# Kernel tuning notes

Measured on AMD Instinct MI355X. Metric: run time of the kernel, lower is better.

Reference implementation:

```python
import jax, jax.numpy as jnp
import numpy as np

B, C, Q, T, D = 16, 6, 256, 256, 256
NUM_IDS = 300
IMG_H = IMG_W = 512


def setup_inputs() -> dict:
    key = jax.random.key(0)
    ks = jax.random.split(key, 8)
    det_tokens = jax.random.normal(ks[0], (B, C, Q, D), jnp.float32)
    det_scores = jax.random.uniform(ks[1], (B, C, Q), jnp.float32)
    det_boxes = jax.random.uniform(ks[2], (B, C, Q, 4), jnp.float32)
    assoc = jax.nn.softmax(jax.random.normal(ks[3], (B, C, Q, T), jnp.float32), axis=-1)
    cam_mask = jax.random.uniform(ks[4], (B, C)) < 0.9
    target_mask = jax.random.uniform(ks[5], (B, C, Q)) < 0.5
    ids = jax.random.randint(ks[6], (B, C, Q), 0, NUM_IDS)
    boxes = jax.random.uniform(ks[7], (B, C, Q, 4), jnp.float32) * IMG_W
    return {"det_tokens": det_tokens, "det_scores": det_scores, "det_boxes": det_boxes,
            "assoc": assoc, "boxes": boxes, "cam_mask": cam_mask,
            "target_mask": target_mask, "ids": ids, "img_h": IMG_H, "img_w": IMG_W}


def _masked_mean(x, m):
    w = m.astype(x.dtype)
    return (x * w).sum() / jnp.maximum(w.sum(), 1.0)


def _pack(ids, target_mask, cam_mask, q_count):
    # Vectorized version of _query_ids_from_targets: stable-compact valid targets
    # to the front of the query axis (preserves original order, as boolean indexing does).
    order = jnp.argsort(jnp.where(target_mask, 0, 1), axis=-1, stable=True)  # valid first
    sids = jnp.take_along_axis(ids, order, axis=-1)[..., :q_count]
    count = target_mask.sum(axis=-1)  # [B,C]
    qvalid = (jnp.arange(q_count)[None, None, :] < count[..., None]) & cam_mask[..., None]
    qids = jnp.where(qvalid, sids, -1)
    return qids, qvalid, order


def reference(det_tokens, det_scores, det_boxes, assoc, boxes, cam_mask, target_mask, ids, img_h, img_w):
    Bq, Cc, Qn, Tn = assoc.shape
    qids, qvalid, order = _pack(ids, target_mask, cam_mask, Qn)

    # det_norm
    det_norm = jnp.mean(det_tokens ** 2)

    # detector supervision (masked BCE on scores + masked L1 on boxes)
    norm = jnp.array([img_w, img_h, img_w, img_h], det_boxes.dtype)
    box_gt = boxes / norm  # [B,C,maxT,4]
    sboxes = jnp.take_along_axis(box_gt, order[..., None], axis=2)[:, :, :Qn]
    obj_target = qvalid.astype(det_scores.dtype)
    box_target = jnp.where(qvalid[..., None], jnp.clip(sboxes, 0.0, 1.0), 0.0)
    p = jnp.clip(det_scores, 1e-6, 1.0 - 1e-6)
    bce = -(obj_target * jnp.log(p) + (1.0 - obj_target) * jnp.log1p(-p))
    cam3 = jnp.broadcast_to(cam_mask[:, :, None], bce.shape)
    score_loss = _masked_mean(bce, cam3)
    box_loss = _masked_mean(jnp.abs(det_boxes - box_target),
                            jnp.broadcast_to(qvalid[..., None], det_boxes.shape))
    det_supervision = score_loss + box_loss

    # assoc entropy (masked by camera validity)
    logp_full = jnp.log(jnp.maximum(assoc, 1e-8))
    entropy = -(logp_full * assoc).sum(-1)  # [B,C,Q]
    assoc_entropy_loss = _masked_mean(entropy, jnp.broadcast_to(cam_mask[:, :, None], entropy.shape))

    # assoc supervised NLL over track slots
    slots = jnp.remainder(jnp.maximum(qids, 0), Tn)  # [B,C,Q]
    nll = -jnp.take_along_axis(logp_full, slots[..., None], axis=-1)[..., 0]
    assoc_pair_loss = _masked_mean(nll, qvalid)

    # cross-view consistency: broadcasted id-equality replaces quadruple python loop
    eq = qids[:, :, None, :, None] == qids[:, None, :, None, :]       # [B,c1,c2,q1,q2]
    pv = qvalid[:, :, None, :, None] & qvalid[:, None, :, None, :]
    tri = jnp.triu(jnp.ones((Cc, Cc), bool), 1)[None, :, :, None, None]  # c1 < c2
    M = (eq & pv & tri).astype(assoc.dtype)
    cnt = M.sum(-1)  # [B,c1,c2,q1]
    peer = jnp.einsum('bcdqp,bdpt->bcdqt', M, assoc) / jnp.maximum(cnt, 1.0)[..., None]
    ref = assoc[:, :, None, :, :]
    term = jnp.mean((ref - peer) ** 2, axis=-1)  # per-pair MSE over track slots
    assoc_consistency = _masked_mean(term, cnt > 0)

    total = det_norm + det_supervision + assoc_entropy_loss + assoc_pair_loss + assoc_consistency
    return total, det_norm, det_supervision, assoc_entropy_loss, assoc_pair_loss, assoc_consistency
```

## Files before the change

### kernel.cpp

```cpp
#include <hip/hip_runtime.h>
#include <math.h>

#define BB 16
#define CC 6
#define QQ 256
#define TT 256
#define DD 256
#define NPAIR 15
#define NBC (BB * CC)
#define BIG_BLOCKS (NBC * 16)
#define CONS_BLOCKS (BB * NPAIR * 4)
#define MAIN_BLOCKS (BIG_BLOCKS + CONS_BLOCKS)


__device__ __forceinline__ float block_sum256(float v, float* s_red) {
    #pragma unroll
    for (int off = 32; off > 0; off >>= 1) v += __shfl_xor(v, off, 64);
    __syncthreads();
    if ((threadIdx.x & 63) == 0) s_red[threadIdx.x >> 6] = v;
    __syncthreads();
    return s_red[0] + s_red[1] + s_red[2] + s_red[3];
}

__device__ __forceinline__ float2 block_sum256x2(float a, float b, float2* s_red2) {
    #pragma unroll
    for (int off = 32; off > 0; off >>= 1) {
        a += __shfl_xor(a, off, 64);
        b += __shfl_xor(b, off, 64);
    }
    __syncthreads();
    if ((threadIdx.x & 63) == 0) s_red2[threadIdx.x >> 6] = make_float2(a, b);
    __syncthreads();
    float2 r;
    r.x = s_red2[0].x + s_red2[1].x + s_red2[2].x + s_red2[3].x;
    r.y = s_red2[0].y + s_red2[1].y + s_red2[2].y + s_red2[3].y;
    return r;
}

__device__ __forceinline__ int read_bool(const void* p, int idx, int fmt) {
    if (fmt == 2) return ((const float*)p)[idx] != 0.0f;
    if (fmt == 1) return ((const unsigned char*)p)[idx] != 0;
    return ((const int*)p)[idx] != 0;
}

__global__ __launch_bounds__(256)
void k_pack(const float* __restrict__ det_scores,
            const float* __restrict__ det_boxes,
            const float* __restrict__ assoc,
            const float* __restrict__ boxes,
            const void* __restrict__ cam_raw,
            const void* __restrict__ tm_raw,
            const int* __restrict__ ids,
            const int* __restrict__ img_h_p,
            const int* __restrict__ img_w_p,
            unsigned char* __restrict__ cam_c,
            int* __restrict__ qids,
            float* __restrict__ packPart) {
    const int bc = blockIdx.x;
    const int t = threadIdx.x;
    const int lane = t & 63, wv = t >> 6;
    __shared__ int s_cf, s_cm, s_wsum[4];
    __shared__ int s_sids[QQ];
    __shared__ float s_red[4];

    if (t == 0) { s_cf = 0; s_cm = 0; }
    __syncthreads();
    {
        uint4 w = ((const uint4*)tm_raw)[t];
        unsigned int u4[4] = {w.x, w.y, w.z, w.w};
        int cf = 0, cm = 0;
        #pragma unroll
        for (int k = 0; k < 4; k++) {
            cf += ((u4[k] >> 24) == 0x3Fu);
            cm += ((u4[k] & 0xFFFFFF00u) != 0u);
        }
        if (cf) atomicAdd(&s_cf, cf);
        if (cm) atomicAdd(&s_cm, cm);
    }
    __syncthreads();
    const int fmt = (s_cf > 16) ? 2 : ((s_cm > 0) ? 1 : 0);

    const int cam = read_bool(cam_raw, bc, fmt);
    const int tm  = read_bool(tm_raw, bc * QQ + t, fmt);
    if (t == 0) cam_c[bc] = (unsigned char)cam;

    int v = tm;
    #pragma unroll
    for (int off = 1; off < 64; off <<= 1) {
        int u = __shfl_up(v, off, 64);
        if (lane >= off) v += u;
    }
    if (lane == 63) s_wsum[wv] = v;
    __syncthreads();
    const int count = s_wsum[0] + s_wsum[1] + s_wsum[2] + s_wsum[3];
    int woff = 0;
    #pragma unroll
    for (int k = 0; k < 3; k++) woff += (k < wv) ? s_wsum[k] : 0;
    const int excl = woff + v - tm;
    const int rank = tm ? excl : (count + (t - excl));

    s_sids[rank] = ids[bc * QQ + t];
    __syncthreads();

    const int j = t;
    const int qv = (j < count) && cam;
    const int qid = qv ? s_sids[j] : -1;
    qids[bc * QQ + j] = qid;

    float score_sum = 0.0f, box_sum = 0.0f, pair_sum = 0.0f;

    if (cam) {
        float p = det_scores[(size_t)bc * QQ + j];
        p = fminf(fmaxf(p, 1e-6f), 1.0f - 1e-6f);
        score_sum = (j < count) ? -__logf(p) : -__logf(1.0f - p);
    }
    if (qv) {
        int slot = qid & (TT - 1);
        float a = assoc[((size_t)bc * QQ + j) * TT + slot];
        pair_sum = -__logf(fmaxf(a, 1e-8f));
    }
    if (tm && cam) {
        const int jj = rank;
        const float iw = (float)img_w_p[0], ih = (float)img_h_p[0];
        const float* bx = boxes + ((size_t)bc * QQ + t) * 4;
        const float* db = det_boxes + ((size_t)bc * QQ + jj) * 4;
        float b0 = fminf(fmaxf(bx[0] / iw, 0.0f), 1.0f);
        float b1 = fminf(fmaxf(bx[1] / ih, 0.0f), 1.0f);
        float b2 = fminf(fmaxf(bx[2] / iw, 0.0f), 1.0f);
        float b3 = fminf(fmaxf(bx[3] / ih, 0.0f), 1.0f);
        box_sum = fabsf(db[0] - b0) + fabsf(db[1] - b1) +
                  fabsf(db[2] - b2) + fabsf(db[3] - b3);
    }

    float vs = block_sum256(score_sum, s_red);
    float vb = block_sum256(box_sum, s_red);
    float vp = block_sum256(pair_sum, s_red);
    if (t == 0) {
        float* row = packPart + bc * 8;
        row[0] = vs; row[1] = vb; row[2] = vp;
        row[3] = cam ? (float)count : 0.0f;
        row[4] = (float)cam;
    }
}

__global__ __launch_bounds__(256)
void k_main(const float4* __restrict__ tok, const float* __restrict__ assoc,
            const unsigned char* __restrict__ cam_c,
            const int* __restrict__ qids,
            float* __restrict__ bigPart, float* __restrict__ consPart) {
    const int blk = blockIdx.x;
    const int t = threadIdx.x, lane = t & 63, wv = t >> 6;
    __shared__ float2 s_red2[4];

    if (blk < BIG_BLOCKS) {
        const int bc = blk >> 4;
        const long base = (long)bc * 16384 + (long)(blk & 15) * 1024 + t;
        const float4* asc = (const float4*)assoc;

        float4 t0 = tok[base], t1 = tok[base + 256],
               t2 = tok[base + 512], t3 = tok[base + 768];
        float4 a0 = asc[base], a1 = asc[base + 256],
               a2 = asc[base + 512], a3 = asc[base + 768];
        const int cam = cam_c[bc];

        float ss = t0.x * t0.x + t0.y * t0.y + t0.z * t0.z + t0.w * t0.w
                 + t1.x * t1.x + t1.y * t1.y + t1.z * t1.z + t1.w * t1.w
                 + t2.x * t2.x + t2.y * t2.y + t2.z * t2.z + t2.w * t2.w
                 + t3.x * t3.x + t3.y * t3.y + t3.z * t3.z + t3.w * t3.w;

        float ent = 0.0f;
        if (cam) {
            ent -= a0.x * __logf(fmaxf(a0.x, 1e-8f)) + a0.y * __logf(fmaxf(a0.y, 1e-8f))
                 + a0.z * __logf(fmaxf(a0.z, 1e-8f)) + a0.w * __logf(fmaxf(a0.w, 1e-8f));
            ent -= a1.x * __logf(fmaxf(a1.x, 1e-8f)) + a1.y * __logf(fmaxf(a1.y, 1e-8f))
                 + a1.z * __logf(fmaxf(a1.z, 1e-8f)) + a1.w * __logf(fmaxf(a1.w, 1e-8f));
            ent -= a2.x * __logf(fmaxf(a2.x, 1e-8f)) + a2.y * __logf(fmaxf(a2.y, 1e-8f))
                 + a2.z * __logf(fmaxf(a2.z, 1e-8f)) + a2.w * __logf(fmaxf(a2.w, 1e-8f));
            ent -= a3.x * __logf(fmaxf(a3.x, 1e-8f)) + a3.y * __logf(fmaxf(a3.y, 1e-8f))
                 + a3.z * __logf(fmaxf(a3.z, 1e-8f)) + a3.w * __logf(fmaxf(a3.w, 1e-8f));
        }
        float2 r = block_sum256x2(ss, ent, s_red2);
        if (t == 0) { bigPart[blk * 2] = r.x; bigPart[blk * 2 + 1] = r.y; }
    } else {
        const int cb = blk - BIG_BLOCKS;
        const int qg = cb & 3;
        const int bp = cb >> 2;
        const int b = bp / NPAIR;
        int pi = bp % NPAIR;
        int c = 0, d = 1;
        {
            int k = pi;
            for (c = 0; c < CC - 1; c++) {
                int span = CC - 1 - c;
                if (k < span) { d = c + 1 + k; break; }
                k -= span;
            }
        }
        __shared__ int s_qc[64];
        __shared__ int s_qd[QQ];
        if (t < 64) s_qc[t] = qids[(b * CC + c) * QQ + qg * 64 + t];
        s_qd[t] = qids[(b * CC + d) * QQ + t];
        __syncthreads();

        const int qd0 = s_qd[lane];
        const int qd1 = s_qd[64 + lane];
        const int qd2 = s_qd[128 + lane];
        const int qd3 = s_qd[192 + lane];
        int idarr[16];
        #pragma unroll
        for (int qi = 0; qi < 16; qi++) idarr[qi] = s_qc[wv * 16 + qi];

        const float4* assoc_c = (const float4*)(assoc + (size_t)(b * CC + c) * QQ * TT);
        const float4* assoc_d = (const float4*)(assoc + (size_t)(b * CC + d) * QQ * TT);

        float tot = 0.0f;
        float nval = 0.0f;
        #pragma unroll 4
        for (int qi = 0; qi < 16; qi++) {
            const int id = idarr[qi];
            if (id < 0) continue;
            unsigned long long m0 = __ballot(qd0 == id);
            unsigned long long m1 = __ballot(qd1 == id);
            unsigned long long m2 = __ballot(qd2 == id);
            unsigned long long m3 = __ballot(qd3 == id);
            int cnt = __popcll(m0) + __popcll(m1) + __popcll(m2) + __popcll(m3);
            if (cnt == 0) continue;
            const int q = qg * 64 + wv * 16 + qi;
            float4 r = assoc_c[(size_t)q * (TT / 4) + lane];
            float ax = 0.0f, ay = 0.0f, az = 0.0f, aw = 0.0f;
            unsigned long long mm[4] = {m0, m1, m2, m3};
            #pragma unroll
            for (int kk = 0; kk < 4; kk++) {
                unsigned long long m = mm[kk];
                while (m) {
                    int p = kk * 64 + __builtin_ctzll(m);
                    m &= m - 1;
                    float4 vv = assoc_d[(size_t)p * (TT / 4) + lane];
                    ax += vv.x; ay += vv.y; az += vv.z; aw += vv.w;
                }
            }
            float inv = 1.0f / (float)cnt;
            float dx = r.x - ax * inv, dy = r.y - ay * inv;
            float dz = r.z - az * inv, dw = r.w - aw * inv;
            tot += dx * dx + dy * dy + dz * dz + dw * dw;
            nval += 1.0f;
        }
        float2 r2 = block_sum256x2(tot, nval, s_red2);
        if (t == 0) {
            consPart[cb * 2] = r2.x * (1.0f / TT);
            consPart[cb * 2 + 1] = r2.y;
        }
    }
}

__global__ __launch_bounds__(256)
void k_fin(const float* __restrict__ packPart, const float2* __restrict__ bigPart,
           const float2* __restrict__ consPart, float* __restrict__ out) {
    const int t = threadIdx.x;
    __shared__ float s_red[4];
    float sc = 0, bx = 0, pr = 0, qv = 0, cm = 0;
    if (t < NBC) {
        const float* row = packPart + t * 8;
        sc = row[0]; bx = row[1]; pr = row[2]; qv = row[3]; cm = row[4];
    }
    float ss = 0, ent = 0;
    #pragma unroll
    for (int k = 0; k < BIG_BLOCKS / 256; k++) {
        float2 v = bigPart[k * 256 + t];
        ss += v.x; ent += v.y;
    }
    float cons = 0, nval = 0;
    for (int i = t; i < CONS_BLOCKS; i += 256) {
        float2 v = consPart[i];
        cons += v.x; nval += v.y;
    }
    sc = block_sum256(sc, s_red);
    bx = block_sum256(bx, s_red);
    pr = block_sum256(pr, s_red);
    qv = block_sum256(qv, s_red);
    cm = block_sum256(cm, s_red);
    ss = block_sum256(ss, s_red);
    ent = block_sum256(ent, s_red);
    cons = block_sum256(cons, s_red);
    nval = block_sum256(nval, s_red);
    if (t == 0) {
        float det_norm = ss / (float)((long)BB * CC * QQ * DD);
        float denom_cam = fmaxf(cm * (float)QQ, 1.0f);
        float score_loss = sc / denom_cam;
        float box_loss = bx / fmaxf(4.0f * qv, 1.0f);
        float det_sup = score_loss + box_loss;
        float ent_loss = ent / denom_cam;
        float pair_loss = pr / fmaxf(qv, 1.0f);
        float cons_loss = cons / fmaxf(nval, 1.0f);
        out[0] = det_norm + det_sup + ent_loss + pair_loss + cons_loss;
        out[1] = det_norm;
        out[2] = det_sup;
        out[3] = ent_loss;
        out[4] = pair_loss;
        out[5] = cons_loss;
    }
}

extern "C" void kernel_launch(void* const* d_in, const int* in_sizes, int n_in,
                              void* d_out, int out_size, void* d_ws, size_t ws_size,
                              hipStream_t stream) {
    const float* det_tokens = (const float*)d_in[0];
    const float* det_scores = (const float*)d_in[1];
    const float* det_boxes  = (const float*)d_in[2];
    const float* assoc      = (const float*)d_in[3];
    const float* boxes      = (const float*)d_in[4];
    const void*  cam_raw    = d_in[5];
    const void*  tm_raw     = d_in[6];
    const int*   ids        = (const int*)d_in[7];
    const int*   img_h      = (const int*)d_in[8];
    const int*   img_w      = (const int*)d_in[9];

    char* ws = (char*)d_ws;
    int* qids            = (int*)(ws + 0);
    unsigned char* cam_c = (unsigned char*)(ws + 98304);
    float* packPart      = (float*)(ws + 98432);
    float* bigPart       = (float*)(ws + 101504);
    float* consPart      = (float*)(ws + 113792);

    k_pack<<<NBC, 256, 0, stream>>>(det_scores, det_boxes, assoc, boxes,
                                    cam_raw, tm_raw, ids, img_h, img_w,
                                    cam_c, qids, packPart);
    k_main<<<MAIN_BLOCKS, 256, 0, stream>>>((const float4*)det_tokens, assoc,
                                            cam_c, qids, bigPart, consPart);
    k_fin<<<1, 256, 0, stream>>>(packPart, (const float2*)bigPart,
                                 (const float2*)consPart, (float*)d_out);
}
```

Baseline: 117.3 us.

## Fuse pack kernel into main kernel by recomputing packed ids per block

Removes the separate k_pack launch. Each consistency block now recomputes the stable compaction of target ids for its two cameras in shared memory, and each big reduction block re-detects the bool format and reads cam_mask itself. The pack losses are computed by extra blocks inside k_main. Big reduction blocks now each process twice as much data (8 per bc instead of 16). This removes one launch and the global qids round trip and dependency, at the cost of redundant prefix-scan work in every consistency block.

Measured after the change: 111.9 us, median of 2. 1.05x faster.

```diff
diff --git a/kernel.cpp b/kernel.cpp
--- a/kernel.cpp
+++ b/kernel.cpp
@@ -8,9 +8,10 @@
 #define DD 256
 #define NPAIR 15
 #define NBC (BB * CC)
-#define BIG_BLOCKS (NBC * 16)
 #define CONS_BLOCKS (BB * NPAIR * 4)
-#define MAIN_BLOCKS (BIG_BLOCKS + CONS_BLOCKS)
+#define PACK_BLOCKS NBC
+#define BIG_BLOCKS (NBC * 8)
+#define MAIN_BLOCKS (CONS_BLOCKS + PACK_BLOCKS + BIG_BLOCKS)
 
 
 __device__ __forceinline__ float block_sum256(float v, float* s_red) {
@@ -43,146 +44,160 @@
     return ((const int*)p)[idx] != 0;
 }
 
+__device__ __forceinline__ int detect_fmt(const void* tm_raw, int* s_cf, int* s_cm) {
+    const int t = threadIdx.x;
+    if (t == 0) { *s_cf = 0; *s_cm = 0; }
+    __syncthreads();
+    uint4 w = ((const uint4*)tm_raw)[t];
+    unsigned int u4[4] = {w.x, w.y, w.z, w.w};
+    int cf = 0, cm = 0;
+    #pragma unroll
+    for (int k = 0; k < 4; k++) {
+        cf += ((u4[k] >> 24) == 0x3Fu);
+        cm += ((u4[k] & 0xFFFFFF00u) != 0u);
+    }
+    if (cf) atomicAdd(s_cf, cf);
+    if (cm) atomicAdd(s_cm, cm);
+    __syncthreads();
+    return (*s_cf > 16) ? 2 : ((*s_cm > 0) ? 1 : 0);
+}
+
+__device__ __forceinline__ int block_pack(const void* tm_raw,
+                                          const int* __restrict__ ids,
+                                          int bc, int fmt, int cam,
+                                          int* s_sids, int* s_wsum,
+                                          int* s_out) {
+    const int t = threadIdx.x, lane = t & 63, wv = t >> 6;
+    const int tm = read_bool(tm_raw, bc * QQ + t, fmt);
+    int v = tm;
+    #pragma unroll
+    for (int off = 1; off < 64; off <<= 1) {
+        int u = __shfl_up(v, off, 64);
+        if (lane >= off) v += u;
+    }
+    if (lane == 63) s_wsum[wv] = v;
+    __syncthreads();
+    const int count = s_wsum[0] + s_wsum[1] + s_wsum[2] + s_wsum[3];
+    int woff = 0;
+    #pragma unroll
+    for (int k = 0; k < 3; k++) woff += (k < wv) ? s_wsum[k] : 0;
+    const int excl = woff + v - tm;
+    const int rank = tm ? excl : (count + (t - excl));
+    s_sids[rank] = ids[bc * QQ + t];
+    __syncthreads();
+    s_out[t] = (t < count && cam) ? s_sids[t] : -1;
+    __syncthreads();
+    return count;
+}
+
 __global__ __launch_bounds__(256)
-void k_pack(const float* __restrict__ det_scores,
+void k_main(const float4* __restrict__ tok,
+            const float* __restrict__ assoc,
+            const float* __restrict__ det_scores,
             const float* __restrict__ det_boxes,
-            const float* __restrict__ assoc,
             const float* __restrict__ boxes,
             const void* __restrict__ cam_raw,
             const void* __restrict__ tm_raw,
             const int* __restrict__ ids,
             const int* __restrict__ img_h_p,
             const int* __restrict__ img_w_p,
-            unsigned char* __restrict__ cam_c,
-            int* __restrict__ qids,
-            float* __restrict__ packPart) {
-    const int bc = blockIdx.x;
-    const int t = threadIdx.x;
-    const int lane = t & 63, wv = t >> 6;
-    __shared__ int s_cf, s_cm, s_wsum[4];
-    __shared__ int s_sids[QQ];
-    __shared__ float s_red[4];
-
-    if (t == 0) { s_cf = 0; s_cm = 0; }
-    __syncthreads();
-    {
-        uint4 w = ((const uint4*)tm_raw)[t];
-        unsigned int u4[4] = {w.x, w.y, w.z, w.w};
-        int cf = 0, cm = 0;
-        #pragma unroll
-        for (int k = 0; k < 4; k++) {
-            cf += ((u4[k] >> 24) == 0x3Fu);
-            cm += ((u4[k] & 0xFFFFFF00u) != 0u);
-        }
-        if (cf) atomicAdd(&s_cf, cf);
-        if (cm) atomicAdd(&s_cm, cm);
-    }
-    __syncthreads();
-    const int fmt = (s_cf > 16) ? 2 : ((s_cm > 0) ? 1 : 0);
-
-    const int cam = read_bool(cam_raw, bc, fmt);
-    const int tm  = read_bool(tm_raw, bc * QQ + t, fmt);
-    if (t == 0) cam_c[bc] = (unsigned char)cam;
-
-    int v = tm;
-    #pragma unroll
-    for (int off = 1; off < 64; off <<= 1) {
-        int u = __shfl_up(v, off, 64);
-        if (lane >= off) v += u;
-    }
-    if (lane == 63) s_wsum[wv] = v;
-    __syncthreads();
-    const int count = s_wsum[0] + s_wsum[1] + s_wsum[2] + s_wsum[3];
-    int woff = 0;
-    #pragma unroll
-    for (int k = 0; k < 3; k++) woff += (k < wv) ? s_wsum[k] : 0;
-    const int excl = woff + v - tm;
-    const int rank = tm ? excl : (count + (t - excl));
-
-    s_sids[rank] = ids[bc * QQ + t];
-    __syncthreads();
-
-    const int j = t;
-    const int qv = (j < count) && cam;
-    const int qid = qv ? s_sids[j] : -1;
-    qids[bc * QQ + j] = qid;
-
-    float score_sum = 0.0f, box_sum = 0.0f, pair_sum = 0.0f;
-
-    if (cam) {
-        float p = det_scores[(size_t)bc * QQ + j];
-        p = fminf(fmaxf(p, 1e-6f), 1.0f - 1e-6f);
-        score_sum = (j < count) ? -__logf(p) : -__logf(1.0f - p);
-    }
-    if (qv) {
-        int slot = qid & (TT - 1);
-        float a = assoc[((size_t)bc * QQ + j) * TT + slot];
-        pair_sum = -__logf(fmaxf(a, 1e-8f));
-    }
-    if (tm && cam) {
-        const int jj = rank;
-        const float iw = (float)img_w_p[0], ih = (float)img_h_p[0];
-        const float* bx = boxes + ((size_t)bc * QQ + t) * 4;
-        const float* db = det_boxes + ((size_t)bc * QQ + jj) * 4;
-        float b0 = fminf(fmaxf(bx[0] / iw, 0.0f), 1.0f);
-        float b1 = fminf(fmaxf(bx[1] / ih, 0.0f), 1.0f);
-        float b2 = fminf(fmaxf(bx[2] / iw, 0.0f), 1.0f);
-        float b3 = fminf(fmaxf(bx[3] / ih, 0.0f), 1.0f);
-        box_sum = fabsf(db[0] - b0) + fabsf(db[1] - b1) +
-                  fabsf(db[2] - b2) + fabsf(db[3] - b3);
-    }
-
-    float vs = block_sum256(score_sum, s_red);
-    float vb = block_sum256(box_sum, s_red);
-    float vp = block_sum256(pair_sum, s_red);
-    if (t == 0) {
-        float* row = packPart + bc * 8;
-        row[0] = vs; row[1] = vb; row[2] = vp;
-        row[3] = cam ? (float)count : 0.0f;
-        row[4] = (float)cam;
-    }
-}
-
-__global__ __launch_bounds__(256)
-void k_main(const float4* __restrict__ tok, const float* __restrict__ assoc,
-            const unsigned char* __restrict__ cam_c,
-            const int* __restrict__ qids,
-            float* __restrict__ bigPart, float* __restrict__ consPart) {
+            float* __restrict__ packPart,
+            float* __restrict__ bigPart,
+            float* __restrict__ consPart) {
     const int blk = blockIdx.x;
     const int t = threadIdx.x, lane = t & 63, wv = t >> 6;
+    __shared__ int s_cf, s_cm;
     __shared__ float2 s_red2[4];
 
-    if (blk < BIG_BLOCKS) {
-        const int bc = blk >> 4;
-        const long base = (long)bc * 16384 + (long)(blk & 15) * 1024 + t;
+    if (blk >= CONS_BLOCKS + PACK_BLOCKS) {
+        const int bb = blk - (CONS_BLOCKS + PACK_BLOCKS);
+        const int bc = bb >> 3;
+        const long base = (long)bc * 16384 + (long)(bb & 7) * 2048 + t;
         const float4* asc = (const float4*)assoc;
-
-        float4 t0 = tok[base], t1 = tok[base + 256],
-               t2 = tok[base + 512], t3 = tok[base + 768];
-        float4 a0 = asc[base], a1 = asc[base + 256],
-               a2 = asc[base + 512], a3 = asc[base + 768];
-        const int cam = cam_c[bc];
-
-        float ss = t0.x * t0.x + t0.y * t0.y + t0.z * t0.z + t0.w * t0.w
-                 + t1.x * t1.x + t1.y * t1.y + t1.z * t1.z + t1.w * t1.w
-                 + t2.x * t2.x + t2.y * t2.y + t2.z * t2.z + t2.w * t2.w
-                 + t3.x * t3.x + t3.y * t3.y + t3.z * t3.z + t3.w * t3.w;
-
-        float ent = 0.0f;
+        const int fmt = detect_fmt(tm_raw, &s_cf, &s_cm);
+        const int cam = read_bool(cam_raw, bc, fmt);
+
+        float ss = 0.0f, ent = 0.0f;
+        #pragma unroll
+        for (int h = 0; h < 2; h++) {
+            const long o = base + h * 1024;
+            float4 t0 = tok[o], t1 = tok[o + 256], t2 = tok[o + 512], t3 = tok[o + 768];
+            float4 a0 = asc[o], a1 = asc[o + 256], a2 = asc[o + 512], a3 = asc[o + 768];
+            ss += t0.x * t0.x + t0.y * t0.y + t0.z * t0.z + t0.w * t0.w
+                + t1.x * t1.x + t1.y * t1.y + t1.z * t1.z + t1.w * t1.w
+                + t2.x * t2.x + t2.y * t2.y + t2.z * t2.z + t2.w * t2.w
+                + t3.x * t3.x + t3.y * t3.y + t3.z * t3.z + t3.w * t3.w;
+            if (cam) {
+                ent -= a0.x * __logf(fmaxf(a0.x, 1e-8f)) + a0.y * __logf(fmaxf(a0.y, 1e-8f))
+                     + a0.z * __logf(fmaxf(a0.z, 1e-8f)) + a0.w * __logf(fmaxf(a0.w, 1e-8f));
+                ent -= a1.x * __logf(fmaxf(a1.x, 1e-8f)) + a1.y * __logf(fmaxf(a1.y, 1e-8f))
+                     + a1.z * __logf(fmaxf(a1.z, 1e-8f)) + a1.w * __logf(fmaxf(a1.w, 1e-8f));
+                ent -= a2.x * __logf(fmaxf(a2.x, 1e-8f)) + a2.y * __logf(fmaxf(a2.y, 1e-8f))
+                     + a2.z * __logf(fmaxf(a2.z, 1e-8f)) + a2.w * __logf(fmaxf(a2.w, 1e-8f));
+                ent -= a3.x * __logf(fmaxf(a3.x, 1e-8f)) + a3.y * __logf(fmaxf(a3.y, 1e-8f))
+                     + a3.z * __logf(fmaxf(a3.z, 1e-8f)) + a3.w * __logf(fmaxf(a3.w, 1e-8f));
+            }
+        }
+        float2 r = block_sum256x2(ss, ent, s_red2);
+        if (t == 0) { bigPart[bb * 2] = r.x; bigPart[bb * 2 + 1] = r.y; }
+
+    } else if (blk >= CONS_BLOCKS) {
+        const int bc = blk - CONS_BLOCKS;
+        __shared__ int s_sids[QQ], s_qid[QQ], s_wsum[4];
+        const int fmt = detect_fmt(tm_raw, &s_cf, &s_cm);
+        const int cam = read_bool(cam_raw, bc, fmt);
+        const int count = block_pack(tm_raw, ids, bc, fmt, cam, s_sids, s_wsum, s_qid);
+        const int tm = read_bool(tm_raw, bc * QQ + t, fmt);
+        int v = tm;
+        #pragma unroll
+        for (int off = 1; off < 64; off <<= 1) {
+            int u = __shfl_up(v, off, 64);
+            if (lane >= off) v += u;
+        }
+        int woff = 0;
+        #pragma unroll
+        for (int k = 0; k < 3; k++) woff += (k < wv) ? s_wsum[k] : 0;
+        const int excl = woff + v - tm;
+        const int rank = tm ? excl : (count + (t - excl));
+
+        const int j = t;
+        const int qv = (j < count) && cam;
+        const int qid = s_qid[j];
+
+        float score_sum = 0.0f, box_sum = 0.0f, pair_sum = 0.0f;
         if (cam) {
-            ent -= a0.x * __logf(fmaxf(a0.x, 1e-8f)) + a0.y * __logf(fmaxf(a0.y, 1e-8f))
-                 + a0.z * __logf(fmaxf(a0.z, 1e-8f)) + a0.w * __logf(fmaxf(a0.w, 1e-8f));
-            ent -= a1.x * __logf(fmaxf(a1.x, 1e-8f)) + a1.y * __logf(fmaxf(a1.y, 1e-8f))
-                 + a1.z * __logf(fmaxf(a1.z, 1e-8f)) + a1.w * __logf(fmaxf(a1.w, 1e-8f));
-            ent -= a2.x * __logf(fmaxf(a2.x, 1e-8f)) + a2.y * __logf(fmaxf(a2.y, 1e-8f))
-                 + a2.z * __logf(fmaxf(a2.z, 1e-8f)) + a2.w * __logf(fmaxf(a2.w, 1e-8f));
-            ent -= a3.x * __logf(fmaxf(a3.x, 1e-8f)) + a3.y * __logf(fmaxf(a3.y, 1e-8f))
-                 + a3.z * __logf(fmaxf(a3.z, 1e-8f)) + a3.w * __logf(fmaxf(a3.w, 1e-8f));
-        }
-        float2 r = block_sum256x2(ss, ent, s_red2);
-        if (t == 0) { bigPart[blk * 2] = r.x; bigPart[blk * 2 + 1] = r.y; }
+            float p = det_scores[(size_t)bc * QQ + j];
+            p = fminf(fmaxf(p, 1e-6f), 1.0f - 1e-6f);
+            score_sum = (j < count) ? -__logf(p) : -__logf(1.0f - p);
+        }
+        if (qv) {
+            int slot = qid & (TT - 1);
+            float a = assoc[((size_t)bc * QQ + j) * TT + slot];
+            pair_sum = -__logf(fmaxf(a, 1e-8f));
+        }
+        if (tm && cam) {
+            const int jj = rank;
+            const float iw = (float)img_w_p[0], ih = (float)img_h_p[0];
+            const float* bx = boxes + ((size_t)bc * QQ + t) * 4;
+            const float* db = det_boxes + ((size_t)bc * QQ + jj) * 4;
+            float b0 = fminf(fmaxf(bx[0] / iw, 0.0f), 1.0f);
+            float b1 = fminf(fmaxf(bx[1] / ih, 0.0f), 1.0f);
+            float b2 = fminf(fmaxf(bx[2] / iw, 0.0f), 1.0f);
+            float b3 = fminf(fmaxf(bx[3] / ih, 0.0f), 1.0f);
+            box_sum = fabsf(db[0] - b0) + fabsf(db[1] - b1) +
+                      fabsf(db[2] - b2) + fabsf(db[3] - b3);
+        }
+        float2 r1 = block_sum256x2(score_sum, box_sum, s_red2);
+        float2 r2 = block_sum256x2(pair_sum, 0.0f, s_red2);
+        if (t == 0) {
+            float* row = packPart + bc * 8;
+            row[0] = r1.x; row[1] = r1.y; row[2] = r2.x;
+            row[3] = cam ? (float)count : 0.0f;
+            row[4] = (float)cam;
+        }
+
     } else {
-        const int cb = blk - BIG_BLOCKS;
+        const int cb = blk;
         const int qg = cb & 3;
         const int bp = cb >> 2;
         const int b = bp / NPAIR;
@@ -196,11 +211,12 @@
                 k -= span;
             }
         }
-        __shared__ int s_qc[64];
-        __shared__ int s_qd[QQ];
-        if (t < 64) s_qc[t] = qids[(b * CC + c) * QQ + qg * 64 + t];
-        s_qd[t] = qids[(b * CC + d) * QQ + t];
-        __syncthreads();
+        __shared__ int s_sids[QQ], s_qc[QQ], s_qd[QQ], s_wsum[4];
+        const int fmt = detect_fmt(tm_raw, &s_cf, &s_cm);
+        const int cam_c = read_bool(cam_raw, b * CC + c, fmt);
+        const int cam_d = read_bool(cam_raw, b * CC + d, fmt);
+        block_pack(tm_raw, ids, b * CC + c, fmt, cam_c, s_sids, s_wsum, s_qc);
+        block_pack(tm_raw, ids, b * CC + d, fmt, cam_d, s_sids, s_wsum, s_qd);
 
         const int qd0 = s_qd[lane];
         const int qd1 = s_qd[64 + lane];
@@ -208,13 +224,12 @@
         const int qd3 = s_qd[192 + lane];
         int idarr[16];
         #pragma unroll
-        for (int qi = 0; qi < 16; qi++) idarr[qi] = s_qc[wv * 16 + qi];
+        for (int qi = 0; qi < 16; qi++) idarr[qi] = s_qc[qg * 64 + wv * 16 + qi];
 
         const float4* assoc_c = (const float4*)(assoc + (size_t)(b * CC + c) * QQ * TT);
         const float4* assoc_d = (const float4*)(assoc + (size_t)(b * CC + d) * QQ * TT);
 
-        float tot = 0.0f;
-        float nval = 0.0f;
+        float tot = 0.0f, nval = 0.0f;
         #pragma unroll 4
         for (int qi = 0; qi < 16; qi++) {
             const int id = idarr[qi];
@@ -316,17 +331,14 @@
     const int*   img_w      = (const int*)d_in[9];
 
     char* ws = (char*)d_ws;
-    int* qids            = (int*)(ws + 0);
-    unsigned char* cam_c = (unsigned char*)(ws + 98304);
-    float* packPart      = (float*)(ws + 98432);
-    float* bigPart       = (float*)(ws + 101504);
-    float* consPart      = (float*)(ws + 113792);
-
-    k_pack<<<NBC, 256, 0, stream>>>(det_scores, det_boxes, assoc, boxes,
-                                    cam_raw, tm_raw, ids, img_h, img_w,
-                                    cam_c, qids, packPart);
+    float* packPart = (float*)(ws + 0);
+    float* bigPart  = (float*)(ws + 4096);
+    float* consPart = (float*)(ws + 16384);
+
     k_main<<<MAIN_BLOCKS, 256, 0, stream>>>((const float4*)det_tokens, assoc,
-                                            cam_c, qids, bigPart, consPart);
+                                            det_scores, det_boxes, boxes,
+                                            cam_raw, tm_raw, ids, img_h, img_w,
+                                            packPart, bigPart, consPart);
     k_fin<<<1, 256, 0, stream>>>(packPart, (const float2*)bigPart,
                                  (const float2*)consPart, (float*)d_out);
 }
```
